# Optimization experiments

Measured on AMD Instinct MI355X. Metric: run time of the kernel, lower is better.

Reference implementation:

```python
import jax, jax.numpy as jnp
import numpy as np

DIM = 256
HID = 256
EPS = 1e-5

def _layernorm(x, g, b):
    mu = jnp.mean(x, axis=-1, keepdims=True)
    var = jnp.mean(jnp.square(x - mu), axis=-1, keepdims=True)
    return (x - mu) * jax.lax.rsqrt(var + EPS) * g + b

def setup_inputs() -> dict:
    key = jax.random.key(0)
    ks = jax.random.split(key, 6)
    B, N = 2, 512
    x = jax.random.normal(ks[0], (B, N, DIM), dtype=jnp.float32)
    mask = jax.random.randint(ks[1], (B, N), 0, 2).astype(jnp.bool_)
    s_in = 1.0 / np.sqrt(DIM)
    s_h = 1.0 / np.sqrt(HID)
    return {
        "x": x,
        "mask": mask,
        "ln_g": jnp.ones((DIM,), jnp.float32),
        "ln_b": jnp.zeros((DIM,), jnp.float32),
        "Wl": jax.random.uniform(ks[2], (DIM, HID), jnp.float32, -s_in, s_in),
        "bl": jnp.zeros((HID,), jnp.float32),
        "Wo": jax.random.uniform(ks[3], (HID, HID), jnp.float32, -s_h, s_h),
        "bo": jnp.zeros((HID,), jnp.float32),
        "lno_g": jnp.ones((HID,), jnp.float32),
        "lno_b": jnp.zeros((HID,), jnp.float32),
    }

def reference(x, mask, ln_g, ln_b, Wl, bl, Wo, bo, lno_g, lno_b):
    # x: [B, N, D], mask: [B, N] bool
    xn = _layernorm(x, ln_g, ln_b)
    left = xn @ Wl + bl                                  # [B, N, H]
    outer = left[:, :, None, :] * left[:, None, :, :]    # [B, N, N, H]
    m2 = (mask[:, :, None] & mask[:, None, :])[..., None]  # [B, N, N, 1]
    outer = jnp.where(m2, outer, 0.0)
    h = _layernorm(jax.nn.gelu(outer, approximate=False), lno_g, lno_b)
    return h @ Wo + bo                                   # [B, N, N, H]
```

## Files before the change

kernel.cpp:

```cpp
#include <hip/hip_runtime.h>
#include <stdint.h>

#define DIM 256
#define HID 256
#define NSEQ 512
#define NB 2
#define EPS 1e-5f

typedef __attribute__((ext_vector_type(4))) float f32x4;
typedef __attribute__((ext_vector_type(4))) short bf16x4;
typedef __attribute__((ext_vector_type(8))) short bf16x8;

#define DIAG_BLOCKS 512
#define BATCH_BLOCKS 2304

__device__ __forceinline__ unsigned short f2bf(float f) {
    unsigned int u = __float_as_uint(f);
    u += 0x7fffu + ((u >> 16) & 1u);
    return (unsigned short)(u >> 16);
}

__device__ __forceinline__ float bfval(float f) {
    return __uint_as_float((unsigned)f2bf(f) << 16);
}

__device__ __forceinline__ float gelu_fast(float x) {
    const float z  = x * 0.7071067811865476f;
    const float az = fabsf(z);
    const float t  = __builtin_amdgcn_rcpf(fmaf(0.3275911f, az, 1.0f));
    float p = fmaf(1.061405429f, t, -1.453152027f);
    p = fmaf(p, t,  1.421413741f);
    p = fmaf(p, t, -0.284496736f);
    p = fmaf(p, t,  0.254829592f);
    p = p * t;
    const float e = __builtin_amdgcn_exp2f(az * az * -1.4426950408889634f);
    float erfv = fmaf(-p, e, 1.0f);
    erfv = copysignf(erfv, z);
    return 0.5f * x * (1.0f + erfv);
}

__device__ __forceinline__ int pairpos(int k) {
    return ((k >> 5) << 5) + (((k >> 2) & 3) << 3) + (((k >> 4) & 1) << 2) + (k & 3);
}

__global__ __launch_bounds__(256) void prep_kernel(
    const float* __restrict__ x, const void* __restrict__ mask,
    const float* __restrict__ ln_g, const float* __restrict__ ln_b,
    const float* __restrict__ Wl, const float* __restrict__ bl,
    const float* __restrict__ Wo, const float* __restrict__ lno_b,
    const float* __restrict__ bo,
    float* __restrict__ lm, unsigned short* __restrict__ woTp,
    int* __restrict__ maskr, float* __restrict__ cst)
{
    const int row = blockIdx.x;
    const int t = threadIdx.x;
    const int lane = t & 63, w = t >> 6;
    __shared__ float xs[DIM];
    __shared__ float red[8];
    __shared__ int bad_s[4];

    {
        const int v = ((const int*)mask)[t];
        unsigned long long bm = __ballot((v & ~1) != 0);
        if (lane == 0) bad_s[w] = (bm != 0ull) ? 1 : 0;
    }

    float v = x[row * DIM + t];
    float s = v, ss = v * v;
    #pragma unroll
    for (int o = 32; o; o >>= 1) { s += __shfl_xor(s, o); ss += __shfl_xor(ss, o); }
    if (lane == 0) { red[w] = s; red[4 + w] = ss; }
    __syncthreads();
    s  = red[0] + red[1] + red[2] + red[3];
    ss = red[4] + red[5] + red[6] + red[7];
    const float mu  = s * (1.0f / DIM);
    const float var = ss * (1.0f / DIM) - mu * mu;
    const float rs  = rsqrtf(var + EPS);
    xs[t] = (v - mu) * rs * ln_g[t] + ln_b[t];
    __syncthreads();

    float acc = bl[t];
    #pragma unroll 4
    for (int k = 0; k < DIM; k += 4) {
        float4 xv = *(const float4*)&xs[k];
        acc = fmaf(xv.x, Wl[(k + 0) * HID + t], acc);
        acc = fmaf(xv.y, Wl[(k + 1) * HID + t], acc);
        acc = fmaf(xv.z, Wl[(k + 2) * HID + t], acc);
        acc = fmaf(xv.w, Wl[(k + 3) * HID + t], acc);
    }
    const int packed = bad_s[0] | bad_s[1] | bad_s[2] | bad_s[3];
    const int mv = packed ? (int)((const unsigned char*)mask)[row]
                          : ((const int*)mask)[row];
    lm[row * HID + t] = mv ? acc : 0.0f;
    if (t == 0) maskr[row] = mv;

    if (row < HID) {
        woTp[row * HID + pairpos(t)] = f2bf(Wo[t * HID + row]);
    }
    if (row == 0) {
        float c = bo[t];
        for (int k = 0; k < HID; ++k)
            c = fmaf(bfval(lno_b[k]), bfval(Wo[k * HID + t]), c);
        cst[t] = c;
    }
}

__global__ __launch_bounds__(512) void outer_kernel(
    const float* __restrict__ lm, const unsigned short* __restrict__ woTp,
    const float* __restrict__ lno_g, const float* __restrict__ lno_b,
    const float* __restrict__ bo, const int* __restrict__ maskr,
    const float* __restrict__ cst, float* __restrict__ out)
{
    int blk = (int)blockIdx.x;
    int b = 0;
    if (blk >= BATCH_BLOCKS) { b = 1; blk -= BATCH_BLOCKS; }
    int i, jt, mirror;
    if (blk < DIAG_BLOCKS) {
        i = blk; jt = i >> 6; mirror = 0;
    } else {
        const int r2 = blk - DIAG_BLOCKS;
        const int p  = r2 >> 6;
        const int il = r2 & 63;
        int bi = 0, start = 0;
        #pragma unroll
        for (int bb = 0; bb < 7; ++bb) {
            const int s = bb * 7 - (bb * (bb - 1)) / 2;
            if (p >= s) { bi = bb; start = s; }
        }
        const int bj = bi + 1 + (p - start);
        i = bi * 64 + il;
        jt = bj;
        mirror = 1;
    }
    const int j0  = jt * 64;
    const int t    = threadIdx.x;
    const int lane = t & 63;
    const int w    = t >> 6;
    const size_t base = (size_t)(b * NSEQ + i) * NSEQ * HID;

    if (maskr[b * NSEQ + i] == 0) {
        const f32x4 c = *(const f32x4*)&cst[lane * 4];
        #pragma unroll
        for (int r = 0; r < 8; ++r) {
            const int j = j0 + w * 8 + r;
            *(f32x4*)&out[base + (size_t)j * HID + lane * 4] = c;
            if (mirror)
                *(f32x4*)&out[((size_t)(b * NSEQ + j) * NSEQ + i) * HID + lane * 4] = c;
        }
        return;
    }

    __shared__ __align__(16) unsigned char ybuf[64 * 512];

    const float4 li4 = *(const float4*)&lm[(size_t)(b * NSEQ + i) * HID + lane * 4];
    const float4 g4  = *(const float4*)&lno_g[lane * 4];
    const float4 bb4 = *(const float4*)&lno_b[lane * 4];

    const int mvl = maskr[b * NSEQ + j0 + lane];
    const unsigned long long livemask = __ballot(mvl != 0);

    const int wrb = ((lane >> 3) << 6) + ((lane & 3) << 4) + (((lane >> 2) & 1) << 3);

    const uint2 ucst = make_uint2(
        ((unsigned)f2bf(bb4.y) << 16) | (unsigned)f2bf(bb4.x),
        ((unsigned)f2bf(bb4.w) << 16) | (unsigned)f2bf(bb4.z));

    #pragma unroll 4
    for (int r = 0; r < 8; ++r) {
        const int rl = w * 8 + r;
        const int j  = j0 + rl;
        const int off = rl * 512 + (wrb ^ ((rl & 7) << 4));
        if (!((livemask >> rl) & 1ull)) {
            *(uint2*)&ybuf[off] = ucst;
            continue;
        }
        float4 lj4 = *(const float4*)&lm[(size_t)(b * NSEQ + j) * HID + lane * 4];
        float4 p;
        p.x = gelu_fast(li4.x * lj4.x);
        p.y = gelu_fast(li4.y * lj4.y);
        p.z = gelu_fast(li4.z * lj4.z);
        p.w = gelu_fast(li4.w * lj4.w);
        float s  = p.x + p.y + p.z + p.w;
        float ss = p.x * p.x + p.y * p.y + p.z * p.z + p.w * p.w;
        #pragma unroll
        for (int o = 32; o; o >>= 1) { s += __shfl_xor(s, o); ss += __shfl_xor(ss, o); }
        const float mu  = s * (1.0f / HID);
        const float var = ss * (1.0f / HID) - mu * mu;
        const float rs  = rsqrtf(var + EPS);
        const float y0 = (p.x - mu) * rs * g4.x + bb4.x;
        const float y1 = (p.y - mu) * rs * g4.y + bb4.y;
        const float y2 = (p.z - mu) * rs * g4.z + bb4.z;
        const float y3 = (p.w - mu) * rs * g4.w + bb4.w;
        const unsigned int u0 = ((unsigned)f2bf(y1) << 16) | (unsigned)f2bf(y0);
        const unsigned int u1 = ((unsigned)f2bf(y3) << 16) | (unsigned)f2bf(y2);
        *(uint2*)&ybuf[off] = make_uint2(u0, u1);
    }
    __syncthreads();

    const int n0  = w * 32;
    const int l15 = lane & 15;
    const int q   = lane >> 4;

    f32x4 acc[4][2];
    #pragma unroll
    for (int mi = 0; mi < 4; ++mi)
        #pragma unroll
        for (int nh = 0; nh < 2; ++nh)
            acc[mi][nh] = (f32x4){0.f, 0.f, 0.f, 0.f};

#if !__has_builtin(__builtin_amdgcn_mfma_f32_16x16x16bf16_1k)
    #pragma unroll
    for (int mi = 0; mi < 4; ++mi)
        #pragma unroll
        for (int nh = 0; nh < 2; ++nh)
            asm volatile("" : "+v"(acc[mi][nh]));
    asm volatile("s_nop 1");
#endif

    #pragma unroll
    for (int kk2 = 0; kk2 < 8; ++kk2) {
        const int pb = kk2 * 64 + q * 16;
        bf16x8 a8[4], b8[2];
        #pragma unroll
        for (int mi = 0; mi < 4; ++mi) {
            const int rowm = mi * 16 + l15;
            a8[mi] = *(const bf16x8*)&ybuf[rowm * 512 + (pb ^ ((rowm & 7) << 4))];
        }
        #pragma unroll
        for (int nh = 0; nh < 2; ++nh) {
            const int col = n0 + nh * 16 + l15;
            b8[nh] = *(const bf16x8*)&woTp[col * HID + kk2 * 32 + q * 8];
        }
        #pragma unroll
        for (int mi = 0; mi < 4; ++mi) {
            const bf16x4 alo = __builtin_shufflevector(a8[mi], a8[mi], 0, 1, 2, 3);
            const bf16x4 ahi = __builtin_shufflevector(a8[mi], a8[mi], 4, 5, 6, 7);
            #pragma unroll
            for (int nh = 0; nh < 2; ++nh) {
                const bf16x4 blo = __builtin_shufflevector(b8[nh], b8[nh], 0, 1, 2, 3);
                const bf16x4 bhi = __builtin_shufflevector(b8[nh], b8[nh], 4, 5, 6, 7);
#if __has_builtin(__builtin_amdgcn_mfma_f32_16x16x16bf16_1k)
                acc[mi][nh] = __builtin_amdgcn_mfma_f32_16x16x16bf16_1k(
                    blo, alo, acc[mi][nh], 0, 0, 0);
                acc[mi][nh] = __builtin_amdgcn_mfma_f32_16x16x16bf16_1k(
                    bhi, ahi, acc[mi][nh], 0, 0, 0);
#else
                asm volatile("v_mfma_f32_16x16x16_bf16 %0, %1, %2, %0"
                             : "+v"(acc[mi][nh]) : "v"(blo), "v"(alo));
                asm volatile("v_mfma_f32_16x16x16_bf16 %0, %1, %2, %0"
                             : "+v"(acc[mi][nh]) : "v"(bhi), "v"(ahi));
#endif
            }
        }
    }

#if !__has_builtin(__builtin_amdgcn_mfma_f32_16x16x16bf16_1k)
    asm volatile("s_nop 7");
    asm volatile("s_nop 7");
    #pragma unroll
    for (int mi = 0; mi < 4; ++mi)
        #pragma unroll
        for (int nh = 0; nh < 2; ++nh)
            asm volatile("" : "+v"(acc[mi][nh]));
#endif

    #pragma unroll
    for (int mi = 0; mi < 4; ++mi) {
        const int j = j0 + mi * 16 + l15;
        const size_t prow = base + (size_t)j * HID;
        const size_t mrow = ((size_t)(b * NSEQ + j) * NSEQ + i) * HID;
        #pragma unroll
        for (int nh = 0; nh < 2; ++nh) {
            const int h0 = n0 + nh * 16 + q * 4;
            const float4 bo4 = *(const float4*)&bo[h0];
            f32x4 o;
            o[0] = acc[mi][nh][0] + bo4.x;
            o[1] = acc[mi][nh][1] + bo4.y;
            o[2] = acc[mi][nh][2] + bo4.z;
            o[3] = acc[mi][nh][3] + bo4.w;
            *(f32x4*)&out[prow + h0] = o;
            if (mirror)
                *(f32x4*)&out[mrow + h0] = o;
        }
    }
}

extern "C" void kernel_launch(void* const* d_in, const int* in_sizes, int n_in,
                              void* d_out, int out_size, void* d_ws, size_t ws_size,
                              hipStream_t stream) {
    (void)in_sizes; (void)n_in; (void)out_size; (void)ws_size;
    const float* x     = (const float*)d_in[0];
    const void*  mask  = d_in[1];
    const float* ln_g  = (const float*)d_in[2];
    const float* ln_b  = (const float*)d_in[3];
    const float* Wl    = (const float*)d_in[4];
    const float* bl    = (const float*)d_in[5];
    const float* Wo    = (const float*)d_in[6];
    const float* bo    = (const float*)d_in[7];
    const float* lno_g = (const float*)d_in[8];
    const float* lno_b = (const float*)d_in[9];

    char* ws = (char*)d_ws;
    float*          lm    = (float*)ws;
    unsigned short* woTp  = (unsigned short*)(ws + (size_t)NB * NSEQ * HID * 4);
    int*            maskr = (int*)(ws + (size_t)NB * NSEQ * HID * 4 + HID * HID * 2);
    float*          cst   = (float*)(ws + (size_t)NB * NSEQ * HID * 4 + HID * HID * 2
                                        + NB * NSEQ * 4);

    prep_kernel<<<NB * NSEQ, 256, 0, stream>>>(x, mask, ln_g, ln_b, Wl, bl, Wo,
                                               lno_b, bo, lm, woTp, maskr, cst);
    outer_kernel<<<NB * BATCH_BLOCKS, 512, 0, stream>>>(
        lm, woTp, lno_g, lno_b, bo, maskr, cst, (float*)d_out);
}
```

Before: 149.5 us.

## Prefetch Wo fragments before LayerNorm and reorder GEMM loop per row tile

Loads all 16 bf16x8 Wo^T fragments into registers at kernel start, before the GELU/LayerNorm stage, so their global-memory latency overlaps that stage instead of sitting inside the MFMA loop. The GEMM loop is also restructured so the outer loop runs over the four 16-row tiles, each with only two accumulators, and the stores for that tile are issued right after its MFMAs. This cuts accumulator registers and lets stores of one tile overlap the MFMAs of the next. In exchange, 64 VGPRs stay live across the whole elementwise stage, and each tile's MFMA chain now depends serially on its single A load.

After: 155.0 us. 3.7% more time.

```diff
diff --git a/kernel.cpp b/kernel.cpp
--- a/kernel.cpp
+++ b/kernel.cpp
@@ -152,6 +152,18 @@
 
     __shared__ __align__(16) unsigned char ybuf[64 * 512];
 
+    const int n0  = w * 32;
+    const int l15 = lane & 15;
+    const int q   = lane >> 4;
+
+    bf16x8 b8[16];
+    #pragma unroll
+    for (int kk2 = 0; kk2 < 8; ++kk2)
+        #pragma unroll
+        for (int nh = 0; nh < 2; ++nh)
+            b8[kk2 * 2 + nh] =
+                *(const bf16x8*)&woTp[(n0 + nh * 16 + l15) * HID + kk2 * 32 + q * 8];
+
     const float4 li4 = *(const float4*)&lm[(size_t)(b * NSEQ + i) * HID + lane * 4];
     const float4 g4  = *(const float4*)&lno_g[lane * 4];
     const float4 bb4 = *(const float4*)&lno_b[lane * 4];
@@ -197,76 +209,52 @@
     }
     __syncthreads();
 
-    const int n0  = w * 32;
-    const int l15 = lane & 15;
-    const int q   = lane >> 4;
-
-    f32x4 acc[4][2];
     #pragma unroll
-    for (int mi = 0; mi < 4; ++mi)
-        #pragma unroll
-        for (int nh = 0; nh < 2; ++nh)
-            acc[mi][nh] = (f32x4){0.f, 0.f, 0.f, 0.f};
+    for (int mi = 0; mi < 4; ++mi) {
+        const int rowm  = mi * 16 + l15;
+        const int rbyte = rowm * 512;
+        const int swz   = (rowm & 7) << 4;
+
+        f32x4 acc[2];
+        acc[0] = (f32x4){0.f, 0.f, 0.f, 0.f};
+        acc[1] = (f32x4){0.f, 0.f, 0.f, 0.f};
 
 #if !__has_builtin(__builtin_amdgcn_mfma_f32_16x16x16bf16_1k)
-    #pragma unroll
-    for (int mi = 0; mi < 4; ++mi)
-        #pragma unroll
-        for (int nh = 0; nh < 2; ++nh)
-            asm volatile("" : "+v"(acc[mi][nh]));
-    asm volatile("s_nop 1");
+        asm volatile("" : "+v"(acc[0]), "+v"(acc[1]));
+        asm volatile("s_nop 1");
 #endif
 
-    #pragma unroll
-    for (int kk2 = 0; kk2 < 8; ++kk2) {
-        const int pb = kk2 * 64 + q * 16;
-        bf16x8 a8[4], b8[2];
-        #pragma unroll
-        for (int mi = 0; mi < 4; ++mi) {
-            const int rowm = mi * 16 + l15;
-            a8[mi] = *(const bf16x8*)&ybuf[rowm * 512 + (pb ^ ((rowm & 7) << 4))];
-        }
-        #pragma unroll
-        for (int nh = 0; nh < 2; ++nh) {
-            const int col = n0 + nh * 16 + l15;
-            b8[nh] = *(const bf16x8*)&woTp[col * HID + kk2 * 32 + q * 8];
-        }
-        #pragma unroll
-        for (int mi = 0; mi < 4; ++mi) {
-            const bf16x4 alo = __builtin_shufflevector(a8[mi], a8[mi], 0, 1, 2, 3);
-            const bf16x4 ahi = __builtin_shufflevector(a8[mi], a8[mi], 4, 5, 6, 7);
+        #pragma unroll
+        for (int kk2 = 0; kk2 < 8; ++kk2) {
+            const bf16x8 a8 = *(const bf16x8*)&ybuf[rbyte + ((kk2 * 64 + q * 16) ^ swz)];
+            const bf16x4 alo = __builtin_shufflevector(a8, a8, 0, 1, 2, 3);
+            const bf16x4 ahi = __builtin_shufflevector(a8, a8, 4, 5, 6, 7);
             #pragma unroll
             for (int nh = 0; nh < 2; ++nh) {
-                const bf16x4 blo = __builtin_shufflevector(b8[nh], b8[nh], 0, 1, 2, 3);
-                const bf16x4 bhi = __builtin_shufflevector(b8[nh], b8[nh], 4, 5, 6, 7);
+                const bf16x8 bf8 = b8[kk2 * 2 + nh];
+                const bf16x4 blo = __builtin_shufflevector(bf8, bf8, 0, 1, 2, 3);
+                const bf16x4 bhi = __builtin_shufflevector(bf8, bf8, 4, 5, 6, 7);
 #if __has_builtin(__builtin_amdgcn_mfma_f32_16x16x16bf16_1k)
-                acc[mi][nh] = __builtin_amdgcn_mfma_f32_16x16x16bf16_1k(
-                    blo, alo, acc[mi][nh], 0, 0, 0);
-                acc[mi][nh] = __builtin_amdgcn_mfma_f32_16x16x16bf16_1k(
-                    bhi, ahi, acc[mi][nh], 0, 0, 0);
+                acc[nh] = __builtin_amdgcn_mfma_f32_16x16x16bf16_1k(
+                    blo, alo, acc[nh], 0, 0, 0);
+                acc[nh] = __builtin_amdgcn_mfma_f32_16x16x16bf16_1k(
+                    bhi, ahi, acc[nh], 0, 0, 0);
 #else
                 asm volatile("v_mfma_f32_16x16x16_bf16 %0, %1, %2, %0"
-                             : "+v"(acc[mi][nh]) : "v"(blo), "v"(alo));
+                             : "+v"(acc[nh]) : "v"(blo), "v"(alo));
                 asm volatile("v_mfma_f32_16x16x16_bf16 %0, %1, %2, %0"
-                             : "+v"(acc[mi][nh]) : "v"(bhi), "v"(ahi));
+                             : "+v"(acc[nh]) : "v"(bhi), "v"(ahi));
 #endif
             }
         }
-    }
 
 #if !__has_builtin(__builtin_amdgcn_mfma_f32_16x16x16bf16_1k)
-    asm volatile("s_nop 7");
-    asm volatile("s_nop 7");
-    #pragma unroll
-    for (int mi = 0; mi < 4; ++mi)
-        #pragma unroll
-        for (int nh = 0; nh < 2; ++nh)
-            asm volatile("" : "+v"(acc[mi][nh]));
+        asm volatile("s_nop 7");
+        asm volatile("s_nop 7");
+        asm volatile("" : "+v"(acc[0]), "+v"(acc[1]));
 #endif
 
-    #pragma unroll
-    for (int mi = 0; mi < 4; ++mi) {
-        const int j = j0 + mi * 16 + l15;
+        const int j = j0 + rowm;
         const size_t prow = base + (size_t)j * HID;
         const size_t mrow = ((size_t)(b * NSEQ + j) * NSEQ + i) * HID;
         #pragma unroll
@@ -274,10 +262,10 @@
             const int h0 = n0 + nh * 16 + q * 4;
             const float4 bo4 = *(const float4*)&bo[h0];
             f32x4 o;
-            o[0] = acc[mi][nh][0] + bo4.x;
-            o[1] = acc[mi][nh][1] + bo4.y;
-            o[2] = acc[mi][nh][2] + bo4.z;
-            o[3] = acc[mi][nh][3] + bo4.w;
+            o[0] = acc[nh][0] + bo4.x;
+            o[1] = acc[nh][1] + bo4.y;
+            o[2] = acc[nh][2] + bo4.z;
+            o[3] = acc[nh][3] + bo4.w;
             *(f32x4*)&out[prow + h0] = o;
             if (mirror)
                 *(f32x4*)&out[mrow + h0] = o;
```
